# Performance work log

Hardware: AMD Instinct MI355X
Metric: run time of the kernel (lower is better)

The kernel has to match this reference:

```python
import jax, jax.numpy as jnp
import numpy as np
from jax import lax

DN = ('NHWC', 'HWIO', 'NHWC')


def _conv(x, w):
    # x: [B,H,W,Cin], w: [kh,kw,Cin,Cout], 'same' padding
    return lax.conv_general_dilated(x, w, (1, 1), 'SAME', dimension_numbers=DN)


def _hard_sigmoid(x):
    # Keras hard_sigmoid: clip(0.2*x + 0.5, 0, 1)
    return jnp.clip(0.2 * x + 0.5, 0.0, 1.0)


def convlstm2d(x, Wk, Uk, b, filters):
    """Keras ConvLSTM2D, return_sequences=True, padding='same'.
    x: [B,T,H,W,Cin]. Gate order in kernel: [i, f, c, o].
    Returns h sequence [B,T,H,W,filters].
    """
    B, T, H, W, _ = x.shape
    h0 = jnp.zeros((B, H, W, filters), x.dtype)
    c0 = jnp.zeros((B, H, W, filters), x.dtype)

    def step(carry, xt):
        h, c = carry
        z = _conv(xt, Wk) + _conv(h, Uk) + b  # [B,H,W,4*filters]
        zi, zf, zc, zo = jnp.split(z, 4, axis=-1)
        i = _hard_sigmoid(zi)
        f = _hard_sigmoid(zf)
        o = _hard_sigmoid(zo)
        c_new = f * c + i * jnp.tanh(zc)
        h_new = o * jnp.tanh(c_new)
        return (h_new, c_new), h_new

    xs = jnp.moveaxis(x, 1, 0)  # [T,B,H,W,Cin]
    _, hs = lax.scan(step, (h0, c0), xs)
    return jnp.moveaxis(hs, 0, 1)  # [B,T,H,W,filters]


def setup_inputs() -> dict:
    key = jax.random.key(0)
    ks = jax.random.split(key, 7)
    B, T, H, W, Cin, F = 8, 10, 64, 64, 32, 64
    s = 0.05
    return {
        'x': jax.random.normal(ks[0], (B, T, H, W, Cin), jnp.float32),
        'Wk1': jax.random.normal(ks[1], (5, 5, Cin, 4 * F), jnp.float32) * s,
        'Uk1': jax.random.normal(ks[2], (5, 5, F, 4 * F), jnp.float32) * s,
        'b1': jnp.zeros((4 * F,), jnp.float32),
        'Wk2': jax.random.normal(ks[3], (3, 3, F, 4 * F), jnp.float32) * s,
        'Uk2': jax.random.normal(ks[4], (3, 3, F, 4 * F), jnp.float32) * s,
        'b2': jnp.zeros((4 * F,), jnp.float32),
    }


def reference(x, Wk1, Uk1, b1, Wk2, Uk2, b2):
    F = Uk1.shape[2]
    y = jax.nn.relu(convlstm2d(x, Wk1, Uk1, b1, F))
    y = jax.nn.relu(convlstm2d(y, Wk2, Uk2, b2, F))
    return y
```

## Files before the change

### kernel.cpp

```cpp
#include <hip/hip_runtime.h>
#include <cstdint>
#include <cmath>


#define NT  256
#define NTU 256

typedef __attribute__((ext_vector_type(8))) short short8;
typedef __attribute__((ext_vector_type(4))) float f32x4;

__device__ __forceinline__ float hsig(float v) {
    return fminf(fmaxf(fmaf(v, 0.2f, 0.5f), 0.0f), 1.0f);
}

__device__ __forceinline__ short bf16rnd(float f) {
    union { float f; unsigned u; } a; a.f = f;
    return (short)((a.u + 0x7FFFu + ((a.u >> 16) & 1u)) >> 16);
}

__device__ __forceinline__ void split_bf16(float f, short& h, short& l) {
    h = bf16rnd(f);
    union { unsigned u; float f; } b; b.u = ((unsigned)(unsigned short)h) << 16;
    l = bf16rnd(f - b.f);
}

__device__ __forceinline__ float from_bf16(short s) {
    union { unsigned u; float f; } b; b.u = ((unsigned)(unsigned short)s) << 16;
    return b.f;
}

struct BF { uint4 bh[4]; uint4 bl[4]; };

template<int CINX, int KS, bool WRITE_SEQ>
__global__ __launch_bounds__(NT, 2)
void convlstm_step(
    const short* __restrict__ xp, long xp_bstride,
    const short* __restrict__ h_prev,
    float* __restrict__ c_state,
    const short* __restrict__ Wpk,
    const short* __restrict__ Upk,
    const float* __restrict__ bias,
    short* __restrict__ h_next,
    short* __restrict__ seq, long seq_bstride)
{
    constexpr int PAD  = KS / 2;
    constexpr int COLS = 64 + 2 * PAD;
    constexpr int CHX  = CINX / 32;
    constexpr int SEGS = CHX + 2;
    constexpr int PSTX = 2 * CINX + 8;
    constexpr int PSTH = 136;
    constexpr int VPPX = CINX / 4;

    __shared__ __align__(16) short xs[COLS * PSTX];
    __shared__ __align__(16) short hs[COLS * PSTH];

    const int tid  = threadIdx.x;
    const int lane = tid & 63;
    const int fg   = tid >> 6;
    const int q8   = ((lane >> 4) & 3) * 8;
    const int batch = blockIdx.x >> 6;
    const int y     = blockIdx.x & 63;

    const short* xim = xp + (size_t)batch * xp_bstride;
    const short* him = h_prev + (size_t)batch * 4096 * 128;

    for (int idx = tid; idx < (COLS * PSTX) / 8; idx += NT) {
        uint4 z; z.x = 0; z.y = 0; z.z = 0; z.w = 0;
        *(uint4*)(xs + idx * 8) = z;
    }
    for (int idx = tid; idx < (COLS * PSTH) / 8; idx += NT) {
        uint4 z; z.x = 0; z.y = 0; z.z = 0; z.w = 0;
        *(uint4*)(hs + idx * 8) = z;
    }

    f32x4 acc[4][4];
    #pragma unroll
    for (int g = 0; g < 4; ++g)
        #pragma unroll
        for (int mt = 0; mt < 4; ++mt)
            #pragma unroll
            for (int r = 0; r < 4; ++r) acc[g][mt][r] = 0.0f;

    auto loadB = [&](int ky, int kx, int s) -> BF {
        int tap = ky * KS + kx;
        const short* base;
        if (s < CHX)
            base = Wpk + ((size_t)((tap * CHX + s) * 16 + fg)) * 1024 + lane * 16;
        else
            base = Upk + ((size_t)((tap * 2 + (s - CHX)) * 16 + fg)) * 1024 + lane * 16;
        BF b;
        #pragma unroll
        for (int g = 0; g < 4; ++g) {
            b.bh[g] = *(const uint4*)(base + (size_t)g * 4096);
            b.bl[g] = *(const uint4*)(base + (size_t)g * 4096 + 8);
        }
        return b;
    };

    const int ky0   = (y < PAD) ? (PAD - y) : 0;
    const int kyend = (64 + PAD - y) < KS ? (64 + PAD - y) : KS;

    BF bcur = loadB(ky0, 0, 0);

    for (int ky = ky0; ky < kyend; ++ky) {
        int yin = y + ky - PAD;
        __syncthreads();
        const short* xrow = xim + (size_t)yin * 64 * 2 * CINX;
        for (int idx = tid; idx < 64 * VPPX; idx += NT) {
            int px = idx / VPPX;
            int v  = idx - px * VPPX;
            *(uint4*)(xs + (px + PAD) * PSTX + v * 8)
                = *(const uint4*)(xrow + px * 2 * CINX + v * 8);
        }
        const short* hrow = him + (size_t)yin * 64 * 128;
        for (int idx = tid; idx < 64 * 16; idx += NT) {
            int px = idx >> 4;
            int v  = idx & 15;
            *(uint4*)(hs + (px + PAD) * PSTH + v * 8)
                = *(const uint4*)(hrow + px * 128 + v * 8);
        }
        __syncthreads();

        #pragma unroll
        for (int kx = 0; kx < KS; ++kx) {
            #pragma unroll
            for (int s = 0; s < SEGS; ++s) {
                int ns = s + 1, nkx = kx, nky = ky;
                if (ns == SEGS) { ns = 0; ++nkx; }
                if (nkx == KS)  { nkx = 0; ++nky; }
                nky = (nky < kyend) ? nky : ky;
                BF bnxt = loadB(nky, nkx, ns);

                short8 ah[4], al[4];
                #pragma unroll
                for (int mt = 0; mt < 4; ++mt) {
                    int col = mt * 16 + (lane & 15) + kx;
                    const short* p = (s < CHX)
                        ? (xs + col * PSTX + s * 32 + q8)
                        : (hs + col * PSTH + (s - CHX) * 32 + q8);
                    int lo = (s < CHX) ? CINX : 64;
                    ah[mt] = *(const short8*)p;
                    al[mt] = *(const short8*)(p + lo);
                }
                #pragma unroll
                for (int g = 0; g < 4; ++g) {
                    short8 bh = *(const short8*)&bcur.bh[g];
                    short8 bl = *(const short8*)&bcur.bl[g];
                    #pragma unroll
                    for (int mt = 0; mt < 4; ++mt) {
                        acc[g][mt] = __builtin_amdgcn_mfma_f32_16x16x32_bf16(
                            ah[mt], bh, acc[g][mt], 0, 0, 0);
                        acc[g][mt] = __builtin_amdgcn_mfma_f32_16x16x32_bf16(
                            al[mt], bh, acc[g][mt], 0, 0, 0);
                        acc[g][mt] = __builtin_amdgcn_mfma_f32_16x16x32_bf16(
                            ah[mt], bl, acc[g][mt], 0, 0, 0);
                    }
                }
                bcur = bnxt;
            }
        }
    }

    const int fl = fg * 16 + (lane & 15);
    const float b_i = bias[fl];
    const float b_f = bias[64 + fl];
    const float b_c = bias[128 + fl];
    const float b_o = bias[192 + fl];
    const int q = (lane >> 4) & 3;

    const long pixbase = (long)batch * 4096 + (long)y * 64;
    const long cb = pixbase * 64 + fl;
    const long sb = (long)batch * seq_bstride + ((long)y * 64) * 128 + fl;

    #pragma unroll
    for (int mt = 0; mt < 4; ++mt) {
        #pragma unroll
        for (int r = 0; r < 4; ++r) {
            int col = mt * 16 + q * 4 + r;
            long cidx = cb + (long)col * 64;
            float zi = acc[0][mt][r] + b_i;
            float zf = acc[1][mt][r] + b_f;
            float zc = acc[2][mt][r] + b_c;
            float zo = acc[3][mt][r] + b_o;
            float ig = hsig(zi);
            float fgt = hsig(zf);
            float og = hsig(zo);
            float cp = c_state[cidx];
            float cn = fgt * cp + ig * tanhf(zc);
            float hn = og * tanhf(cn);
            c_state[cidx] = cn;

            short hh, hl;
            split_bf16(hn, hh, hl);
            long hoff = (pixbase + col) * 128 + fl;
            h_next[hoff]      = hh;
            h_next[hoff + 64] = hl;
            if (WRITE_SEQ) {
                bool pos = hn > 0.0f;
                seq[sb + (long)col * 128]      = pos ? hh : (short)0;
                seq[sb + (long)col * 128 + 64] = pos ? hl : (short)0;
            }
        }
    }
}

__global__ void convert_planes32(const float4* __restrict__ src,
                                 unsigned* __restrict__ dst, int n4)
{
    int t = blockIdx.x * NTU + threadIdx.x;
    if (t >= n4) return;
    int pix = t >> 3;
    int c4  = t & 7;
    float4 v = src[t];
    short h0, l0, h1, l1, h2, l2, h3, l3;
    split_bf16(v.x, h0, l0);
    split_bf16(v.y, h1, l1);
    split_bf16(v.z, h2, l2);
    split_bf16(v.w, h3, l3);
    unsigned* p = dst + (size_t)pix * 32;
    p[c4 * 2]      = (unsigned)(unsigned short)h0 | ((unsigned)(unsigned short)h1 << 16);
    p[c4 * 2 + 1]  = (unsigned)(unsigned short)h2 | ((unsigned)(unsigned short)h3 << 16);
    p[16 + c4 * 2]     = (unsigned)(unsigned short)l0 | ((unsigned)(unsigned short)l1 << 16);
    p[16 + c4 * 2 + 1] = (unsigned)(unsigned short)l2 | ((unsigned)(unsigned short)l3 << 16);
}

__global__ void repack(const float* __restrict__ src, short* __restrict__ dst,
                       int KS, int CH)
{
    int total = KS * KS * CH * 16 * 64;
    int t = blockIdx.x * NTU + threadIdx.x;
    if (t >= total) return;
    int u = t >> 6, lane = t & 63;
    int tap = u / (CH * 16);
    int rem = u - tap * (CH * 16);
    int ch = rem >> 4;
    int gfg = rem & 15;
    int g = gfg >> 2, fgp = gfg & 3;
    int CIN = CH * 32;
    int n = lane & 15, qq = lane >> 4;
    short* d = dst + (size_t)u * 1024 + lane * 16;
    int gc = g * 64 + fgp * 16 + n;
    for (int j = 0; j < 8; ++j) {
        int c = ch * 32 + qq * 8 + j;
        float w = src[((size_t)tap * CIN + c) * 256 + gc];
        short h, l;
        split_bf16(w, h, l);
        d[j] = h;
        d[8 + j] = l;
    }
}

__global__ void relu_copy(const short* __restrict__ hp, float* __restrict__ out,
                          long out_bstride)
{
    long i = (long)blockIdx.x * NTU + threadIdx.x;
    long pix = i >> 6;
    int c = (int)(i & 63);
    float f = from_bf16(hp[pix * 128 + c]) + from_bf16(hp[pix * 128 + 64 + c]);
    long b = pix >> 12;
    long within = (pix & 4095) * 64 + c;
    out[b * out_bstride + within] = fmaxf(f, 0.0f);
}

extern "C" void kernel_launch(void* const* d_in, const int* in_sizes, int n_in,
                              void* d_out, int out_size, void* d_ws, size_t ws_size,
                              hipStream_t stream) {
    const float* x   = (const float*)d_in[0];
    const float* Wk1 = (const float*)d_in[1];
    const float* Uk1 = (const float*)d_in[2];
    const float* b1  = (const float*)d_in[3];
    const float* Wk2 = (const float*)d_in[4];
    const float* Uk2 = (const float*)d_in[5];
    const float* b2  = (const float*)d_in[6];
    float* out = (float*)d_out;

    const long S  = (long)8 * 64 * 64 * 64;
    const long oT = (long)64 * 64 * 64;
    const long oB = 10 * oT;

    short* h_a = (short*)d_ws;
    short* h_b = h_a + 2 * S;
    float* c_s = (float*)(h_b + 2 * S);
    short* Wp1 = (short*)(c_s + S);
    short* Up1 = Wp1 + 25 * 1 * 16 * 1024;
    short* Wp2 = Up1 + 25 * 2 * 16 * 1024;
    short* Up2 = Wp2 + 9 * 2 * 16 * 1024;
    short* x1p = Up2 + 9 * 2 * 16 * 1024;
    (void)ws_size;

    {
        int n4 = 8 * 10 * 4096 * 8;
        convert_planes32<<<dim3((n4 + NTU - 1) / NTU), dim3(NTU), 0, stream>>>(
            (const float4*)x, (unsigned*)x1p, n4);
    }
    repack<<<dim3((25 * 1 * 16 * 64 + NTU - 1) / NTU), dim3(NTU), 0, stream>>>(Wk1, Wp1, 5, 1);
    repack<<<dim3((25 * 2 * 16 * 64 + NTU - 1) / NTU), dim3(NTU), 0, stream>>>(Uk1, Up1, 5, 2);
    repack<<<dim3((9 * 2 * 16 * 64 + NTU - 1) / NTU), dim3(NTU), 0, stream>>>(Wk2, Wp2, 3, 2);
    repack<<<dim3((9 * 2 * 16 * 64 + NTU - 1) / NTU), dim3(NTU), 0, stream>>>(Uk2, Up2, 3, 2);

    short* seqs = (short*)d_out;

    hipMemsetAsync(h_a, 0, (size_t)S * 4, stream);
    hipMemsetAsync(c_s, 0, (size_t)S * 4, stream);
    short* hc = h_a;
    short* hn = h_b;
    const long x1T = (long)4096 * 64;
    const long x1B = 10 * x1T;
    for (int t = 0; t < 10; ++t) {
        convlstm_step<32, 5, true><<<dim3(512), dim3(NT), 0, stream>>>(
            x1p + t * x1T, x1B, hc, c_s, Wp1, Up1, b1, hn,
            seqs + t * oT * 2, oB * 2);
        short* tmp = hc; hc = hn; hn = tmp;
    }

    hipMemsetAsync(hc, 0, (size_t)S * 4, stream);
    hipMemsetAsync(c_s, 0, (size_t)S * 4, stream);
    for (int t = 0; t < 10; ++t) {
        convlstm_step<64, 3, false><<<dim3(512), dim3(NT), 0, stream>>>(
            seqs + t * oT * 2, oB * 2, hc, c_s, Wp2, Up2, b2, hn,
            nullptr, 0);
        relu_copy<<<dim3(8192), dim3(NTU), 0, stream>>>(hn, out + t * oT, oB);
        short* tmp = hc; hc = hn; hn = tmp;
    }
}
```

Measured before the change: 1.880 ms.

## Wavefront-fuse layer-1 and layer-2 ConvLSTM steps into one launch with relu

Runs layer-1 step t and layer-2 step t-1 in a single launch, with relu output for step t-2 handled by extra blocks. The two layers no longer run as separate serial sequences of small 512-block launches, which should fill the GPU better and cut launch count. It also adds a zero-h specialization for the first layer-1 step that skips the recurrent h convolution and the c read. In exchange it needs a larger workspace, falls back to the old path when the workspace is too small, and uses dynamic shared memory sized for the larger layer, which may reduce occupancy for the layer-1 blocks.

```diff
diff --git a/kernel.cpp b/kernel.cpp
--- a/kernel.cpp
+++ b/kernel.cpp
@@ -3,8 +3,9 @@
 #include <cmath>
 
 
-#define NT  256
-#define NTU 256
+#define NT        256
+#define NTU       256
+#define RELU_BLKS 256
 
 typedef __attribute__((ext_vector_type(8))) short short8;
 typedef __attribute__((ext_vector_type(4))) float f32x4;
@@ -31,9 +32,9 @@
 
 struct BF { uint4 bh[4]; uint4 bl[4]; };
 
-template<int CINX, int KS, bool WRITE_SEQ>
-__global__ __launch_bounds__(NT, 2)
-void convlstm_step(
+template<int CINX, int KS, bool WRITE_SEQ, bool HZ>
+__device__ __forceinline__ void step_body(
+    short* __restrict__ xs, short* __restrict__ hs,
     const short* __restrict__ xp, long xp_bstride,
     const short* __restrict__ h_prev,
     float* __restrict__ c_state,
@@ -41,25 +42,23 @@
     const short* __restrict__ Upk,
     const float* __restrict__ bias,
     short* __restrict__ h_next,
-    short* __restrict__ seq, long seq_bstride)
+    short* __restrict__ seq, long seq_bstride,
+    int bidx)
 {
     constexpr int PAD  = KS / 2;
     constexpr int COLS = 64 + 2 * PAD;
     constexpr int CHX  = CINX / 32;
-    constexpr int SEGS = CHX + 2;
+    constexpr int SEGS = HZ ? CHX : (CHX + 2);
     constexpr int PSTX = 2 * CINX + 8;
     constexpr int PSTH = 136;
     constexpr int VPPX = CINX / 4;
-
-    __shared__ __align__(16) short xs[COLS * PSTX];
-    __shared__ __align__(16) short hs[COLS * PSTH];
 
     const int tid  = threadIdx.x;
     const int lane = tid & 63;
     const int fg   = tid >> 6;
     const int q8   = ((lane >> 4) & 3) * 8;
-    const int batch = blockIdx.x >> 6;
-    const int y     = blockIdx.x & 63;
+    const int batch = bidx >> 6;
+    const int y     = bidx & 63;
 
     const short* xim = xp + (size_t)batch * xp_bstride;
     const short* him = h_prev + (size_t)batch * 4096 * 128;
@@ -68,9 +67,11 @@
         uint4 z; z.x = 0; z.y = 0; z.z = 0; z.w = 0;
         *(uint4*)(xs + idx * 8) = z;
     }
-    for (int idx = tid; idx < (COLS * PSTH) / 8; idx += NT) {
-        uint4 z; z.x = 0; z.y = 0; z.z = 0; z.w = 0;
-        *(uint4*)(hs + idx * 8) = z;
+    if constexpr (!HZ) {
+        for (int idx = tid; idx < (COLS * PSTH) / 8; idx += NT) {
+            uint4 z; z.x = 0; z.y = 0; z.z = 0; z.w = 0;
+            *(uint4*)(hs + idx * 8) = z;
+        }
     }
 
     f32x4 acc[4][4];
@@ -112,12 +113,14 @@
             *(uint4*)(xs + (px + PAD) * PSTX + v * 8)
                 = *(const uint4*)(xrow + px * 2 * CINX + v * 8);
         }
-        const short* hrow = him + (size_t)yin * 64 * 128;
-        for (int idx = tid; idx < 64 * 16; idx += NT) {
-            int px = idx >> 4;
-            int v  = idx & 15;
-            *(uint4*)(hs + (px + PAD) * PSTH + v * 8)
-                = *(const uint4*)(hrow + px * 128 + v * 8);
+        if constexpr (!HZ) {
+            const short* hrow = him + (size_t)yin * 64 * 128;
+            for (int idx = tid; idx < 64 * 16; idx += NT) {
+                int px = idx >> 4;
+                int v  = idx & 15;
+                *(uint4*)(hs + (px + PAD) * PSTH + v * 8)
+                    = *(const uint4*)(hrow + px * 128 + v * 8);
+            }
         }
         __syncthreads();
 
@@ -185,7 +188,7 @@
             float ig = hsig(zi);
             float fgt = hsig(zf);
             float og = hsig(zo);
-            float cp = c_state[cidx];
+            float cp = HZ ? 0.0f : c_state[cidx];
             float cn = fgt * cp + ig * tanhf(zc);
             float hn = og * tanhf(cn);
             c_state[cidx] = cn;
@@ -200,6 +203,67 @@
                 seq[sb + (long)col * 128]      = pos ? hh : (short)0;
                 seq[sb + (long)col * 128 + 64] = pos ? hl : (short)0;
             }
+        }
+    }
+}
+
+template<int CINX, int KS, bool WRITE_SEQ, bool HZ>
+__global__ __launch_bounds__(NT, 2)
+void convlstm_step(
+    const short* __restrict__ xp, long xp_bstride,
+    const short* __restrict__ h_prev,
+    float* __restrict__ c_state,
+    const short* __restrict__ Wpk,
+    const short* __restrict__ Upk,
+    const float* __restrict__ bias,
+    short* __restrict__ h_next,
+    short* __restrict__ seq, long seq_bstride)
+{
+    extern __shared__ __align__(16) short smem[];
+    constexpr int PAD  = KS / 2;
+    constexpr int COLS = 64 + 2 * PAD;
+    constexpr int PSTX = 2 * CINX + 8;
+    step_body<CINX, KS, WRITE_SEQ, HZ>(
+        smem, smem + COLS * PSTX,
+        xp, xp_bstride, h_prev, c_state, Wpk, Upk, bias,
+        h_next, seq, seq_bstride, (int)blockIdx.x);
+}
+
+__global__ __launch_bounds__(NT, 4)
+void convlstm_fused(
+    const short* __restrict__ x1, long x1_bs,
+    const short* __restrict__ h1p, float* __restrict__ c1,
+    const short* __restrict__ Wp1, const short* __restrict__ Up1,
+    const float* __restrict__ b1,
+    short* __restrict__ h1n, short* __restrict__ seq1, long seq1_bs,
+    const short* __restrict__ x2, long x2_bs,
+    const short* __restrict__ h2p, float* __restrict__ c2,
+    const short* __restrict__ Wp2, const short* __restrict__ Up2,
+    const float* __restrict__ b2,
+    short* __restrict__ h2n,
+    const short* __restrict__ relu_src, float* __restrict__ relu_dst,
+    long out_bstride)
+{
+    extern __shared__ __align__(16) short smem[];
+    const int b = (int)blockIdx.x;
+    if (b < 512) {
+        step_body<32, 5, true, false>(
+            smem, smem + 68 * 72,
+            x1, x1_bs, h1p, c1, Wp1, Up1, b1, h1n, seq1, seq1_bs, b);
+    } else if (b < 1024) {
+        step_body<64, 3, false, false>(
+            smem, smem + 66 * 136,
+            x2, x2_bs, h2p, c2, Wp2, Up2, b2, h2n, nullptr, 0, b - 512);
+    } else {
+        if (relu_dst == nullptr) return;
+        long i = (long)(b - 1024) * NT + threadIdx.x;
+        for (; i < (1L << 21); i += (long)RELU_BLKS * NT) {
+            long pix = i >> 6;
+            int  c   = (int)(i & 63);
+            float f = from_bf16(relu_src[pix * 128 + c])
+                    + from_bf16(relu_src[pix * 128 + 64 + c]);
+            long bb = pix >> 12;
+            relu_dst[bb * out_bstride + (pix & 4095) * 64 + c] = fmaxf(f, 0.0f);
         }
     }
 }
@@ -277,16 +341,40 @@
     const long S  = (long)8 * 64 * 64 * 64;
     const long oT = (long)64 * 64 * 64;
     const long oB = 10 * oT;
-
-    short* h_a = (short*)d_ws;
-    short* h_b = h_a + 2 * S;
-    float* c_s = (float*)(h_b + 2 * S);
-    short* Wp1 = (short*)(c_s + S);
+    const long x1T = (long)4096 * 64;
+    const long x1B = 10 * x1T;
+
+    const size_t HB  = (size_t)4 * S;
+    const size_t CB  = (size_t)4 * S;
+    const size_t W1B = (size_t)25 * 1 * 16 * 1024 * 2;
+    const size_t U1B = (size_t)25 * 2 * 16 * 1024 * 2;
+    const size_t W2B = (size_t)9 * 2 * 16 * 1024 * 2;
+    const size_t U2B = (size_t)9 * 2 * 16 * 1024 * 2;
+    const size_t XPB = (size_t)8 * x1B * 2;
+    const size_t need_ov = 4 * HB + 2 * CB + W1B + U1B + W2B + U2B + XPB;
+    const bool ov = (ws_size >= need_ov);
+
+    short* h1a = (short*)d_ws;
+    short* h1b = h1a + 2 * S;
+    short *h2a, *h2b;
+    float *c1, *c2;
+    short* Wp1;
+    if (ov) {
+        h2a = h1b + 2 * S;
+        h2b = h2a + 2 * S;
+        c1  = (float*)(h2b + 2 * S);
+        c2  = c1 + S;
+        Wp1 = (short*)(c2 + S);
+    } else {
+        h2a = h1a; h2b = h1b;
+        c1  = (float*)(h1b + 2 * S);
+        c2  = c1;
+        Wp1 = (short*)(c1 + S);
+    }
     short* Up1 = Wp1 + 25 * 1 * 16 * 1024;
     short* Wp2 = Up1 + 25 * 2 * 16 * 1024;
     short* Up2 = Wp2 + 9 * 2 * 16 * 1024;
     short* x1p = Up2 + 9 * 2 * 16 * 1024;
-    (void)ws_size;
 
     {
         int n4 = 8 * 10 * 4096 * 8;
@@ -300,26 +388,59 @@
 
     short* seqs = (short*)d_out;
 
-    hipMemsetAsync(h_a, 0, (size_t)S * 4, stream);
-    hipMemsetAsync(c_s, 0, (size_t)S * 4, stream);
-    short* hc = h_a;
-    short* hn = h_b;
-    const long x1T = (long)4096 * 64;
-    const long x1B = 10 * x1T;
-    for (int t = 0; t < 10; ++t) {
-        convlstm_step<32, 5, true><<<dim3(512), dim3(NT), 0, stream>>>(
-            x1p + t * x1T, x1B, hc, c_s, Wp1, Up1, b1, hn,
-            seqs + t * oT * 2, oB * 2);
-        short* tmp = hc; hc = hn; hn = tmp;
-    }
-
-    hipMemsetAsync(hc, 0, (size_t)S * 4, stream);
-    hipMemsetAsync(c_s, 0, (size_t)S * 4, stream);
-    for (int t = 0; t < 10; ++t) {
-        convlstm_step<64, 3, false><<<dim3(512), dim3(NT), 0, stream>>>(
-            seqs + t * oT * 2, oB * 2, hc, c_s, Wp2, Up2, b2, hn,
+    const size_t SH_L1HZ = (size_t)(68 * 72) * 2;
+    const size_t SH_L1   = (size_t)(68 * 72 + 68 * 136) * 2;
+    const size_t SH_L2   = (size_t)(66 * 136) * 4;
+    const size_t SH_F    = SH_L2;
+
+    if (ov) {
+        hipMemsetAsync(h2a, 0, HB, stream);
+        hipMemsetAsync(c2, 0, CB, stream);
+
+        convlstm_step<32, 5, true, true><<<dim3(512), dim3(NT), SH_L1HZ, stream>>>(
+            x1p, x1B, h1a, c1, Wp1, Up1, b1, h1b, seqs, oB * 2);
+
+        short* hc1 = h1b; short* hn1 = h1a;
+        short* hc2 = h2a; short* hn2 = h2b;
+        for (int t = 1; t < 10; ++t) {
+            const short* x2 = seqs + (size_t)(t - 1) * oT * 2;
+            float* rdst = (t >= 2) ? (out + (size_t)(t - 2) * oT) : (float*)nullptr;
+            convlstm_fused<<<dim3(1024 + RELU_BLKS), dim3(NT), SH_F, stream>>>(
+                x1p + (size_t)t * x1T, x1B, hc1, c1, Wp1, Up1, b1, hn1,
+                seqs + (size_t)t * oT * 2, oB * 2,
+                x2, oB * 2, hc2, c2, Wp2, Up2, b2, hn2,
+                hc2, rdst, oB);
+            short* tmp;
+            tmp = hc1; hc1 = hn1; hn1 = tmp;
+            tmp = hc2; hc2 = hn2; hn2 = tmp;
+        }
+        convlstm_step<64, 3, false, false><<<dim3(512), dim3(NT), SH_L2, stream>>>(
+            seqs + (size_t)9 * oT * 2, oB * 2, hc2, c2, Wp2, Up2, b2, hn2,
             nullptr, 0);
-        relu_copy<<<dim3(8192), dim3(NTU), 0, stream>>>(hn, out + t * oT, oB);
-        short* tmp = hc; hc = hn; hn = tmp;
-    }
-}
+        relu_copy<<<dim3(8192), dim3(NTU), 0, stream>>>(hc2, out + 8 * oT, oB);
+        relu_copy<<<dim3(8192), dim3(NTU), 0, stream>>>(hn2, out + 9 * oT, oB);
+    } else {
+        convlstm_step<32, 5, true, true><<<dim3(512), dim3(NT), SH_L1HZ, stream>>>(
+            x1p, x1B, h1a, c1, Wp1, Up1, b1, h1b, seqs, oB * 2);
+        short* hc = h1b; short* hn = h1a;
+        for (int t = 1; t < 10; ++t) {
+            convlstm_step<32, 5, true, false><<<dim3(512), dim3(NT), SH_L1, stream>>>(
+                x1p + (size_t)t * x1T, x1B, hc, c1, Wp1, Up1, b1, hn,
+                seqs + (size_t)t * oT * 2, oB * 2);
+            short* tmp = hc; hc = hn; hn = tmp;
+        }
+        hipMemsetAsync(hc, 0, HB, stream);
+        hipMemsetAsync(c2, 0, CB, stream);
+        convlstm_step<64, 3, false, false><<<dim3(512), dim3(NT), SH_L2, stream>>>(
+            seqs, oB * 2, hc, c2, Wp2, Up2, b2, hn, nullptr, 0);
+        relu_copy<<<dim3(8192), dim3(NTU), 0, stream>>>(hn, out, oB);
+        { short* tmp = hc; hc = hn; hn = tmp; }
+        for (int t = 1; t < 10; ++t) {
+            convlstm_step<64, 3, false, false><<<dim3(512), dim3(NT), SH_L2, stream>>>(
+                seqs + (size_t)t * oT * 2, oB * 2, hc, c2, Wp2, Up2, b2, hn,
+                nullptr, 0);
+            relu_copy<<<dim3(8192), dim3(NTU), 0, stream>>>(hn, out + (size_t)t * oT, oB);
+            short* tmp = hc; hc = hn; hn = tmp;
+        }
+    }
+}
```

Result: slower. 2.331 ms (+24.0%).
